# Kernel optimization log

Hardware: AMD Instinct MI355X
Metric: run time of the kernel (lower is better)

## Reference

```python
import jax, jax.numpy as jnp
import numpy as np

EPS = 1e-5


def _bn_relu(y, g, beta, relu=True):
    # BatchNorm1d in training mode: biased batch stats over (B, V) per channel
    mean = jnp.mean(y, axis=(0, 2), keepdims=True)
    var = jnp.mean((y - mean) ** 2, axis=(0, 2), keepdims=True)
    out = (y - mean) * jax.lax.rsqrt(var + EPS) * g[None, :, None] + beta[None, :, None]
    return jnp.maximum(out, 0.0) if relu else out


def _spiral_conv(x, idx, w, b, g, beta):
    # x: (B,C,V), idx: (V,L) -> gather (B,C,V,L), row-major reshape to (B,C*L,V)
    B, C, V = x.shape
    L = idx.shape[1]
    neigh = x[:, :, idx].reshape(B, C * L, V)
    y = jnp.einsum('om,bmv->bov', w, neigh) + b[None, :, None]
    return _bn_relu(y, g, beta)


def _se(x, w1, w2):
    s = jnp.mean(x, axis=2)                              # (B,C)
    h = jnp.maximum(jnp.einsum('bc,rc->br', s, w1), 0.0)  # (B,r)
    s = jax.nn.sigmoid(jnp.einsum('br,cr->bc', h, w2))   # (B,C)
    return x * s[:, :, None]


def setup_inputs() -> dict:
    key = jax.random.key(0)
    ks = jax.random.split(key, 24)
    B, V, L, H = 2, 16384, 12, 256
    sc = 0.05
    inp = {
        'verts': jax.random.normal(ks[0], (B, V, 3), jnp.float32),
        'spirals': jax.random.randint(ks[1], (4, V, L), 0, V, jnp.int32),
        'enc0_w': jax.random.normal(ks[2], (H, 3 * L), jnp.float32) * sc,
        'enc0_b': jax.random.normal(ks[3], (H,), jnp.float32) * sc,
        'enc0_g': jnp.ones((H,), jnp.float32),
        'enc0_beta': jnp.zeros((H,), jnp.float32),
        'enc_w': jax.random.normal(ks[4], (3, H, H * L), jnp.float32) * sc,
        'enc_b': jax.random.normal(ks[5], (3, H), jnp.float32) * sc,
        'enc_g': jnp.ones((3, H), jnp.float32),
        'enc_beta': jnp.zeros((3, H), jnp.float32),
        'se_w1': jax.random.normal(ks[6], (4, H // 8, H), jnp.float32) * sc,
        'se_w2': jax.random.normal(ks[7], (4, H, H // 8), jnp.float32) * sc,
        'skip_w': jax.random.normal(ks[8], (3, H, 2 * H), jnp.float32) * sc,
        'skip_b': jax.random.normal(ks[9], (3, H), jnp.float32) * sc,
        'dec_w': jax.random.normal(ks[10], (3, H, H * L), jnp.float32) * sc,
        'dec_b': jax.random.normal(ks[11], (3, H), jnp.float32) * sc,
        'dec_g': jnp.ones((3, H), jnp.float32),
        'dec_beta': jnp.zeros((3, H), jnp.float32),
        'cls1_w': jax.random.normal(ks[12], (H // 2, H), jnp.float32) * sc,
        'cls1_b': jax.random.normal(ks[13], (H // 2,), jnp.float32) * sc,
        'cls1_g': jnp.ones((H // 2,), jnp.float32),
        'cls1_beta': jnp.zeros((H // 2,), jnp.float32),
        'cls2_w': jax.random.normal(ks[14], (H // 4, H // 2), jnp.float32) * sc,
        'cls2_b': jax.random.normal(ks[15], (H // 4,), jnp.float32) * sc,
        'cls2_g': jnp.ones((H // 4,), jnp.float32),
        'cls2_beta': jnp.zeros((H // 4,), jnp.float32),
        'cls3_w': jax.random.normal(ks[16], (1, H // 4), jnp.float32) * sc,
        'cls3_b': jax.random.normal(ks[17], (1,), jnp.float32) * sc,
    }
    return inp


def reference(verts, spirals, enc0_w, enc0_b, enc0_g, enc0_beta,
              enc_w, enc_b, enc_g, enc_beta, se_w1, se_w2,
              skip_w, skip_b, dec_w, dec_b, dec_g, dec_beta,
              cls1_w, cls1_b, cls1_g, cls1_beta,
              cls2_w, cls2_b, cls2_g, cls2_beta, cls3_w, cls3_b):
    x = jnp.transpose(verts, (0, 2, 1))  # (B,3,V)
    feats = []
    # encoder: 4 blocks, block0 has no residual (3 != 256)
    for i in range(4):
        if i == 0:
            out = _spiral_conv(x, spirals[0], enc0_w, enc0_b, enc0_g, enc0_beta)
        else:
            out = _spiral_conv(x, spirals[i], enc_w[i - 1], enc_b[i - 1], enc_g[i - 1], enc_beta[i - 1]) + x
        x = _se(out, se_w1[i], se_w2[i])
        feats.append(x)
    # decoder with skip-concat fusion, spirals[2],[1],[0] and feats[2],[1],[0]
    for i in range(3):
        feat = feats[2 - i]
        idx = spirals[2 - i]
        xc = jnp.concatenate([x, feat], axis=1)  # (B,512,V)
        x = jnp.einsum('oc,bcv->bov', skip_w[i], xc) + skip_b[i][None, :, None]
        x = _spiral_conv(x, idx, dec_w[i], dec_b[i], dec_g[i], dec_beta[i]) + x
    # classifier: 1x1 conv stack
    h = _bn_relu(jnp.einsum('oc,bcv->bov', cls1_w, x) + cls1_b[None, :, None], cls1_g, cls1_beta)
    h = _bn_relu(jnp.einsum('oc,bcv->bov', cls2_w, h) + cls2_b[None, :, None], cls2_g, cls2_beta)
    out = jnp.einsum('oc,bcv->bov', cls3_w, h) + cls3_b[None, :, None]  # (B,1,V)
    return out[:, 0, :]  # (B,V)
```

## Files before the change

kernel.cpp:

```cpp
#include <hip/hip_runtime.h>

typedef unsigned short u16;
using f16x8 = __attribute__((ext_vector_type(8))) _Float16;
using f32x4 = __attribute__((ext_vector_type(4))) float;

#define V_N 16384
#define M_N 32768

__device__ __forceinline__ float h2f(u16 u) {
  _Float16 h; __builtin_memcpy(&h, &u, 2); return (float)h;
}
__device__ __forceinline__ u16 f2h(float f) {
  _Float16 h = (_Float16)f; u16 u; __builtin_memcpy(&u, &h, 2); return u;
}

__device__ __forceinline__ void dma16(const u16* g, u16* l) {
  __builtin_amdgcn_global_load_lds(
      (const __attribute__((address_space(1))) void*)(const void*)g,
      (__attribute__((address_space(3))) void*)(void*)l, 16, 0, 0);
}

__global__ __launch_bounds__(256) void perm2_k(const float* __restrict__ w, u16* __restrict__ wp) {
  int o = blockIdx.x & 255, layer = blockIdx.x >> 8;
  int t = threadIdx.x;
  const float* src = w + ((size_t)layer * 256 + o) * 3072;
  u16* dst = wp + (size_t)layer * 786432;
  float2 v[6];
  #pragma unroll
  for (int q = 0; q < 6; ++q) v[q] = *(const float2*)(src + t * 12 + q * 2);
  const float* vf = (const float*)v;
  int lo = t & 31;
  #pragma unroll
  for (int m = 0; m < 12; ++m) {
    int kc = m * 8 + (t >> 5);
    dst[(size_t)kc * 8192 + o * 32 + lo] = f2h(vf[m]);
  }
}

__global__ __launch_bounds__(256) void permfr_k(const float* __restrict__ src, u16* __restrict__ dst,
                                                int O, int K) {
  int i = blockIdx.x * 256 + threadIdx.x;
  if (i >= (K << 8)) return;
  int j = i & 7, lq = (i >> 3) & 3, col = (i >> 5) & 255, kc = i >> 13;
  int k = kc * 32 + lq * 8 + j;
  float v = (col < O) ? src[(size_t)col * K + k] : 0.f;
  dst[i] = f2h(v);
}

__global__ __launch_bounds__(256) void wscale_k(const u16* __restrict__ w, const float* __restrict__ sig,
                                                const float* __restrict__ sigx,
                                                u16* __restrict__ o, int n, int sel) {
  int i = blockIdx.x * 256 + threadIdx.x;
  if (i >= n) return;
  float wv = h2f(w[i]);
  int k = (i >> 13) * 32 + ((i >> 3) & 3) * 8 + (i & 7);
  int c = k & 255;
  #pragma unroll
  for (int b = 0; b < 2; ++b) {
    float s;
    if (sel == 511 && k < 256) s = sigx ? sigx[b * 256 + c] : 1.f;
    else                       s = sig[b * 256 + c];
    o[(long)b * n + i] = f2h(wv * s);
  }
}

__global__ __launch_bounds__(256) void enc0_k(const float* __restrict__ verts, const int* __restrict__ sp,
                                              const float* __restrict__ w0, u16* __restrict__ y) {
  __shared__ float xs[32][36];
  int t = threadIdx.x;
  int r0 = blockIdx.x * 32;
  for (int s = t; s < 32 * 12; s += 256) {
    int row = s / 12, tt = s - row * 12;
    int gr = r0 + row;
    int b = gr >> 14, v = gr & (V_N - 1);
    int j = sp[tt * V_N + v];
    const float* p = verts + ((long)b * V_N + j) * 3;
    xs[row][tt]      = p[0];
    xs[row][12 + tt] = p[1];
    xs[row][24 + tt] = p[2];
  }
  __syncthreads();
  float w[36];
  #pragma unroll
  for (int k = 0; k < 36; ++k) w[k] = w0[t * 36 + k];
  for (int row = 0; row < 32; ++row) {
    float a = 0.f;
    #pragma unroll
    for (int k = 0; k < 36; ++k) a += w[k] * xs[row][k];
    y[(long)(r0 + row) * 256 + t] = f2h(a);
  }
}

template<int CT>
__global__ __launch_bounds__(512, 4) void gemm3_k(
    const u16* __restrict__ P0, const u16* __restrict__ P1, int lda,
    const int* __restrict__ sp, int L,
    const u16* __restrict__ Wt, long wstride,
    u16* __restrict__ Yb, const float* __restrict__ bias, int Ostore,
    float* __restrict__ stats)
{
  constexpr int KC   = CT >> 5;
  constexpr int PH   = (CT == 256) ? 4 : 2;
  constexpr int KCP  = KC / PH;
  constexpr int PROW = 64;
  constexpr int BUFE = 64 * PROW;
  __shared__ __align__(16) u16 lA[3 * BUFE];
  const int tid  = threadIdx.x;
  const int wave = tid >> 6, lane = tid & 63;
  const int wn = wave * 32;
  const int lr = lane & 15, lq = lane >> 4;
  const int nwg = gridDim.x;
  const int wg = (blockIdx.x & 7) * (nwg >> 3) + (blockIdx.x >> 3);
  const int bm = wg * 64;
  const int batch = bm >> 14;
  const int vbase = bm & (V_N - 1);
  const int qrow = lane >> 3;
  const int qchunk = lane & 7;
  const bool gat = (sp != nullptr);
  const long rowb = (long)batch * V_N;
  const u16* Pd1 = P1 ? P1 : P0;
  const u16* Wb = Wt + (long)batch * wstride;
  const int NS = PH * L;

  const u16* bp[2];
  #pragma unroll
  for (int nt = 0; nt < 2; ++nt)
    bp[nt] = Wb + ((long)(wn + nt * 16 + lr) * 4 + lq) * 8;

  auto load_idx = [&](int tap) -> int {
    int v = 0;
    if (gat && lane < 8) v = sp[(long)tap * V_N + vbase + wave * 8 + lane];
    return v;
  };

  auto dma_st = [&](u16* buf, const u16* src, int idxreg, int ph) {
    u16* wb = buf + wave * (8 * PROW);
    int rloc = wave * 8 + qrow;
    long grow;
    if (gat) grow = rowb + (long)__shfl(idxreg, qrow, 64);
    else     grow = bm + rloc;
    const u16* gp = src + grow * lda + ph * PROW + ((qchunk ^ (rloc & 7)) << 3);
    dma16(gp, wb);
  };

  auto loadB = [&](int cb, f16x8 (&tB)[KCP * 2]) {
    #pragma unroll
    for (int kp = 0; kp < KCP; ++kp)
      #pragma unroll
      for (int nt = 0; nt < 2; ++nt)
        tB[kp * 2 + nt] = *(const f16x8*)(bp[nt] + (long)(cb + kp) * 8192);
  };

  f32x4 acc[4][2];
  #pragma unroll
  for (int i = 0; i < 4; ++i)
    #pragma unroll
    for (int j = 0; j < 2; ++j) acc[i][j] = (f32x4){0.f, 0.f, 0.f, 0.f};

  auto compute_st = [&](const u16* buf, const f16x8 (&tB)[KCP * 2]) {
    #pragma unroll
    for (int kp = 0; kp < KCP; ++kp) {
      f16x8 a[4];
      #pragma unroll
      for (int mt = 0; mt < 4; ++mt) {
        int row = mt * 16 + lr;
        a[mt] = *(const f16x8*)(&buf[row * PROW + (((kp * 4 + lq) ^ (row & 7)) << 3)]);
      }
      #pragma unroll
      for (int mt = 0; mt < 4; ++mt)
        #pragma unroll
        for (int nt = 0; nt < 2; ++nt)
          acc[mt][nt] = __builtin_amdgcn_mfma_f32_16x16x32_f16(a[mt], tB[kp * 2 + nt], acc[mt][nt], 0, 0, 0);
    }
  };

  f16x8 tA[KCP * 2], tB2[KCP * 2];

  auto adv = [&](int& l, int& ph) { if (++l == L) { l = 0; ++ph; } };
  int lB = 0, phB = 0; adv(lB, phB);
  int lD = lB, phD = phB; adv(lD, phD);
  int lI = lD; { int pT = phD; int lT = lI; adv(lT, pT); lI = lT; }
  int idxN;

  {
    int i0 = load_idx(0);
    int i1 = load_idx(lB);
    idxN = load_idx(lD);
    dma_st(lA, P0, i0, 0);
    if (NS > 1) {
      const u16* s1 = (!gat && lB > 0) ? Pd1 : P0;
      dma_st(lA + BUFE, s1, i1, phB);
    }
    __builtin_amdgcn_sched_barrier(0);
    loadB(0, tA);
    __builtin_amdgcn_sched_barrier(0);
  }

  auto stage = [&](int s, f16x8 (&tCur)[KCP * 2], f16x8 (&tNxt)[KCP * 2]) {
    if (s + 1 < NS) asm volatile("s_waitcnt vmcnt(5)" ::: "memory");
    else            asm volatile("s_waitcnt vmcnt(0)" ::: "memory");
    asm volatile("s_waitcnt lgkmcnt(0)" ::: "memory");
    __builtin_amdgcn_s_barrier();
    __builtin_amdgcn_sched_barrier(0);
    if (s + 1 < NS) loadB(lB * KC + phB * KCP, tNxt);
    __builtin_amdgcn_sched_barrier(0);
    int idxT = 0;
    if (gat && s + 3 < NS) idxT = load_idx(lI);
    if (s + 2 < NS) {
      const u16* srcD = (!gat && lD > 0) ? Pd1 : P0;
      dma_st(lA + ((s + 2) % 3) * BUFE, srcD, idxN, phD);
    }
    __builtin_amdgcn_sched_barrier(0);
    compute_st(lA + (s % 3) * BUFE, tCur);
    adv(lB, phB); adv(lD, phD); if (++lI == L) lI = 0;
    idxN = idxT;
  };

  for (int s = 0; s < NS; s += 2) {
    stage(s, tA, tB2);
    stage(s + 1, tB2, tA);
  }

  #pragma unroll
  for (int nt = 0; nt < 2; ++nt) {
    int col = wn + nt * 16 + lr;
    if (col < Ostore) {
      float bv = bias ? bias[col] : 0.f;
      float s1 = 0.f, s2 = 0.f;
      #pragma unroll
      for (int mt = 0; mt < 4; ++mt) {
        #pragma unroll
        for (int rg = 0; rg < 4; ++rg) {
          int row = bm + mt * 16 + lq * 4 + rg;
          float v = acc[mt][nt][rg] + bv;
          Yb[(long)row * Ostore + col] = f2h(v);
          s1 += v; s2 += v * v;
        }
      }
      if (stats) {
        s1 += __shfl_xor(s1, 16); s1 += __shfl_xor(s1, 32);
        s2 += __shfl_xor(s2, 16); s2 += __shfl_xor(s2, 32);
        if (lq == 0) {
          atomicAdd(&stats[col], s1);
          atomicAdd(&stats[Ostore + col], s2);
        }
      }
    }
  }
}

__global__ __launch_bounds__(256) void stats2_k(const u16* __restrict__ y, float* __restrict__ st) {
  __shared__ float s1L[256], s2L[256];
  int tid = threadIdx.x;
  int ci = (tid & 63) * 4;
  int r0 = blockIdx.x * 64 + (tid >> 6);
  float a1[4] = {0,0,0,0}, a2[4] = {0,0,0,0};
  for (int it = 0; it < 16; ++it) {
    long i = ((long)r0 + it * 4) * 256 + ci;
    uint2 pv = *(const uint2*)(y + i);
    float v0 = h2f((u16)(pv.x & 0xffff)), v1 = h2f((u16)(pv.x >> 16));
    float v2 = h2f((u16)(pv.y & 0xffff)), v3 = h2f((u16)(pv.y >> 16));
    a1[0] += v0; a1[1] += v1; a1[2] += v2; a1[3] += v3;
    a2[0] += v0*v0; a2[1] += v1*v1; a2[2] += v2*v2; a2[3] += v3*v3;
  }
  s1L[tid] = 0.f; s2L[tid] = 0.f;
  __syncthreads();
  #pragma unroll
  for (int j = 0; j < 4; ++j) { atomicAdd(&s1L[ci + j], a1[j]); atomicAdd(&s2L[ci + j], a2[j]); }
  __syncthreads();
  atomicAdd(&st[tid], s1L[tid]);
  atomicAdd(&st[256 + tid], s2L[tid]);
}

__global__ __launch_bounds__(256) void bnrelu2_k(
    const u16* __restrict__ y, const float* __restrict__ st,
    const float* __restrict__ g, const float* __restrict__ be,
    const u16* __restrict__ resid, const float* __restrict__ rscale,
    u16* __restrict__ ob, float* __restrict__ ses, int O)
{
  __shared__ float sL[256];
  int tid = threadIdx.x;
  int tpr = O >> 2;
  int rpi = 256 / tpr;
  int ci = (tid & (tpr - 1)) * 4;
  int row0 = blockIdx.x * (rpi * 16);
  int r0 = row0 + (tid / tpr);
  int b = row0 >> 14;
  float mean[4], sc[4], sh[4], rs[4];
  #pragma unroll
  for (int j = 0; j < 4; ++j) {
    int c = ci + j;
    float m = st[c] * (1.f / 32768.f);
    float var = st[O + c] * (1.f / 32768.f) - m * m;
    mean[j] = m;
    sc[j] = rsqrtf(fmaxf(var, 0.f) + 1e-5f) * g[c];
    sh[j] = be[c];
    rs[j] = rscale ? rscale[b * 256 + c] : 1.f;
  }
  float ss[4] = {0,0,0,0};
  for (int it = 0; it < 16; ++it) {
    long i = ((long)r0 + (long)it * rpi) * O + ci;
    uint2 pv = *(const uint2*)(y + i);
    float v[4];
    v[0] = fmaxf((h2f((u16)(pv.x & 0xffff)) - mean[0]) * sc[0] + sh[0], 0.f);
    v[1] = fmaxf((h2f((u16)(pv.x >> 16))    - mean[1]) * sc[1] + sh[1], 0.f);
    v[2] = fmaxf((h2f((u16)(pv.y & 0xffff)) - mean[2]) * sc[2] + sh[2], 0.f);
    v[3] = fmaxf((h2f((u16)(pv.y >> 16))    - mean[3]) * sc[3] + sh[3], 0.f);
    if (resid) {
      uint2 rv = *(const uint2*)(resid + i);
      v[0] += h2f((u16)(rv.x & 0xffff)) * rs[0]; v[1] += h2f((u16)(rv.x >> 16)) * rs[1];
      v[2] += h2f((u16)(rv.y & 0xffff)) * rs[2]; v[3] += h2f((u16)(rv.y >> 16)) * rs[3];
    }
    uint2 pk;
    pk.x = (unsigned)f2h(v[0]) | ((unsigned)f2h(v[1]) << 16);
    pk.y = (unsigned)f2h(v[2]) | ((unsigned)f2h(v[3]) << 16);
    *(uint2*)(ob + i) = pk;
    #pragma unroll
    for (int j = 0; j < 4; ++j) ss[j] += v[j];
  }
  if (ses) {
    sL[tid] = 0.f;
    __syncthreads();
    #pragma unroll
    for (int j = 0; j < 4; ++j) atomicAdd(&sL[ci + j], ss[j]);
    __syncthreads();
    atomicAdd(&ses[b * O + tid], sL[tid]);
  }
}

__global__ void se_k(const float* __restrict__ ses, const float* __restrict__ w1,
                     const float* __restrict__ w2, float* __restrict__ sig)
{
  __shared__ float s[256];
  __shared__ float h[32];
  int b = blockIdx.x, t = threadIdx.x;
  s[t] = ses[b * 256 + t] * (1.f / 16384.f);
  __syncthreads();
  if (t < 32) {
    float a = 0.f;
    for (int c = 0; c < 256; ++c) a += w1[t * 256 + c] * s[c];
    h[t] = fmaxf(a, 0.f);
  }
  __syncthreads();
  float a = 0.f;
  #pragma unroll
  for (int r = 0; r < 32; ++r) a += w2[t * 32 + r] * h[r];
  sig[b * 256 + t] = 1.f / (1.f + expf(-a));
}

__global__ __launch_bounds__(256) void cls3_k(const u16* __restrict__ h2, const float* __restrict__ w,
                                              const float* __restrict__ b, float* __restrict__ out)
{
  __shared__ float ws[64];
  int t = threadIdx.x;
  if (t < 64) ws[t] = w[t];
  __syncthreads();
  int r = blockIdx.x * 256 + t;
  const u16* p = h2 + (long)r * 64;
  float a = b[0];
  #pragma unroll
  for (int c = 0; c < 64; ++c) a += ws[c] * h2f(p[c]);
  out[r] = a;
}

extern "C" void kernel_launch(void* const* d_in, const int* in_sizes, int n_in,
                              void* d_out, int out_size, void* d_ws, size_t ws_size,
                              hipStream_t stream)
{
  (void)in_sizes; (void)n_in; (void)out_size; (void)ws_size;
  const float* verts   = (const float*)d_in[0];
  const int*   spirals = (const int*)d_in[1];
  const float* enc0_w  = (const float*)d_in[2];
  const float* enc0_g  = (const float*)d_in[4];
  const float* enc0_be = (const float*)d_in[5];
  const float* enc_w   = (const float*)d_in[6];
  const float* enc_g   = (const float*)d_in[8];
  const float* enc_be  = (const float*)d_in[9];
  const float* se_w1   = (const float*)d_in[10];
  const float* se_w2   = (const float*)d_in[11];
  const float* skip_w  = (const float*)d_in[12];
  const float* skip_b  = (const float*)d_in[13];
  const float* dec_w   = (const float*)d_in[14];
  const float* dec_g   = (const float*)d_in[16];
  const float* dec_be  = (const float*)d_in[17];
  const float* cls1_w  = (const float*)d_in[18];
  const float* cls1_g  = (const float*)d_in[20];
  const float* cls1_be = (const float*)d_in[21];
  const float* cls2_w  = (const float*)d_in[22];
  const float* cls2_g  = (const float*)d_in[24];
  const float* cls2_be = (const float*)d_in[25];
  const float* cls3_w  = (const float*)d_in[26];
  const float* cls3_b  = (const float*)d_in[27];

  char* p = (char*)d_ws;
  auto alloc = [&](size_t n) { char* q = p; p += (n + 255) & ~(size_t)255; return q; };
  u16* wpe     = (u16*)alloc((size_t)6 * 256 * 3072 * 2);
  u16* wpe_s   = (u16*)alloc((size_t)3 * 2 * 256 * 3072 * 2);
  u16* skip_wb = (u16*)alloc((size_t)3 * 256 * 512 * 2);
  u16* skip_s  = (u16*)alloc((size_t)3 * 2 * 256 * 512 * 2);
  u16* cls1_wb = (u16*)alloc((size_t)256 * 256 * 2);
  u16* wp6     = (u16*)alloc((size_t)256 * 128 * 2);
  float* stats = (float*)alloc(2048);
  float* sesum = (float*)alloc(2048);
  float* sig   = (float*)alloc(4 * 2048);
  u16* out0 = (u16*)alloc((size_t)M_N * 256 * 2);
  u16* out1 = (u16*)alloc((size_t)M_N * 256 * 2);
  u16* out2 = (u16*)alloc((size_t)M_N * 256 * 2);
  u16* ct   = (u16*)alloc((size_t)M_N * 256 * 2);
  u16* tb   = (u16*)alloc((size_t)M_N * 256 * 2);
  u16* xd   = (u16*)alloc((size_t)M_N * 256 * 2);
  u16* outs[4] = {out0, out1, out2, ct};
  const size_t WENC = (size_t)256 * 3072;
  const size_t WSKP = (size_t)256 * 512;

  perm2_k<<<768, 256, 0, stream>>>(enc_w, wpe);
  perm2_k<<<768, 256, 0, stream>>>(dec_w, wpe + (size_t)3 * WENC);
  for (int s = 0; s < 3; ++s)
    permfr_k<<<512, 256, 0, stream>>>(skip_w + (size_t)s * 256 * 512,
                                      skip_wb + (size_t)s * WSKP, 256, 512);
  permfr_k<<<256, 256, 0, stream>>>(cls1_w, cls1_wb, 128, 256);
  permfr_k<<<128, 256, 0, stream>>>(cls2_w, wp6, 64, 128);

  hipMemsetAsync(stats, 0, 4096, stream);
  enc0_k<<<1024, 256, 0, stream>>>(verts, spirals, enc0_w, ct);
  stats2_k<<<512, 256, 0, stream>>>(ct, stats);
  bnrelu2_k<<<512, 256, 0, stream>>>(ct, stats, enc0_g, enc0_be, nullptr, nullptr, out0, sesum, 256);
  se_k<<<2, 256, 0, stream>>>(sesum, se_w1, se_w2, sig);

  for (int i = 1; i < 4; ++i) {
    wscale_k<<<3072, 256, 0, stream>>>(wpe + (size_t)(i - 1) * WENC, sig + (i - 1) * 512, nullptr,
                                       wpe_s + (size_t)(i - 1) * 2 * WENC, (int)WENC, 255);
    hipMemsetAsync(stats, 0, 4096, stream);
    gemm3_k<256><<<512, 512, 0, stream>>>(outs[i - 1], nullptr, 256,
                                          spirals + (size_t)i * V_N * 12, 12,
                                          wpe_s + (size_t)(i - 1) * 2 * WENC, (long)WENC,
                                          ct, nullptr, 256, stats);
    bnrelu2_k<<<512, 256, 0, stream>>>(ct, stats, enc_g + (i - 1) * 256, enc_be + (i - 1) * 256,
                                       outs[i - 1], sig + (i - 1) * 512, outs[i], sesum, 256);
    se_k<<<2, 256, 0, stream>>>(sesum, se_w1 + (size_t)i * 32 * 256,
                                se_w2 + (size_t)i * 256 * 32, sig + i * 512);
  }

  for (int i = 0; i < 3; ++i) {
    wscale_k<<<512, 256, 0, stream>>>(skip_wb + (size_t)i * WSKP, sig + (2 - i) * 512,
                                      (i == 0) ? (sig + 3 * 512) : nullptr,
                                      skip_s + (size_t)i * 2 * WSKP, (int)WSKP, 511);
    gemm3_k<256><<<512, 512, 0, stream>>>((i == 0) ? ct : xd, outs[2 - i], 256, nullptr, 2,
                                          skip_s + (size_t)i * 2 * WSKP, (long)WSKP,
                                          tb, skip_b + i * 256, 256, nullptr);
    hipMemsetAsync(stats, 0, 4096, stream);
    gemm3_k<256><<<512, 512, 0, stream>>>(tb, nullptr, 256,
                                          spirals + (size_t)(2 - i) * V_N * 12, 12,
                                          wpe + (size_t)(3 + i) * WENC, 0,
                                          outs[2 - i], nullptr, 256, stats);
    bnrelu2_k<<<512, 256, 0, stream>>>(outs[2 - i], stats, dec_g + i * 256, dec_be + i * 256,
                                       tb, nullptr, xd, nullptr, 256);
  }

  hipMemsetAsync(stats, 0, 4096, stream);
  gemm3_k<256><<<512, 512, 0, stream>>>(xd, nullptr, 256, nullptr, 1,
                                        cls1_wb, 0, ct, nullptr, 128, stats);
  bnrelu2_k<<<256, 256, 0, stream>>>(ct, stats, cls1_g, cls1_be, nullptr, nullptr, ct, nullptr, 128);
  hipMemsetAsync(stats, 0, 4096, stream);
  gemm3_k<128><<<512, 512, 0, stream>>>(ct, nullptr, 128, nullptr, 1,
                                        wp6, 0, tb, nullptr, 64, stats);
  bnrelu2_k<<<128, 256, 0, stream>>>(tb, stats, cls2_g, cls2_be, nullptr, nullptr, tb, nullptr, 64);
  cls3_k<<<128, 256, 0, stream>>>(tb, cls3_w, cls3_b, (float*)d_out);
}
```

Baseline: 884.5 us.

## Pair taps per GEMM stage, fuse SE and BN stats, drop memsets

The GEMM now processes two spiral taps per pipeline stage, giving each barrier twice the work and fewer stages. It loads the B fragments inline per stage, precomputes the LDS offsets and raises wave priority around the MFMA bursts. BN statistics for enc0 move into enc0_k, and the SE MLP is folded into bnrelu2_k through a last-block counter. Per-layer stats buffers replace the repeated memsets, cutting launches and serialisation. In exchange the larger LDS buffers may lower occupancy, and the inline B loads are no longer prefetched a stage ahead, which can expose global latency.

```diff
diff --git a/kernel.cpp b/kernel.cpp
--- a/kernel.cpp
+++ b/kernel.cpp
@@ -65,7 +65,8 @@
 }
 
 __global__ __launch_bounds__(256) void enc0_k(const float* __restrict__ verts, const int* __restrict__ sp,
-                                              const float* __restrict__ w0, u16* __restrict__ y) {
+                                              const float* __restrict__ w0, u16* __restrict__ y,
+                                              float* __restrict__ st) {
   __shared__ float xs[32][36];
   int t = threadIdx.x;
   int r0 = blockIdx.x * 32;
@@ -83,15 +84,21 @@
   float w[36];
   #pragma unroll
   for (int k = 0; k < 36; ++k) w[k] = w0[t * 36 + k];
+  float s1 = 0.f, s2 = 0.f;
   for (int row = 0; row < 32; ++row) {
     float a = 0.f;
     #pragma unroll
     for (int k = 0; k < 36; ++k) a += w[k] * xs[row][k];
-    y[(long)(r0 + row) * 256 + t] = f2h(a);
-  }
-}
-
-template<int CT>
+    u16 h = f2h(a);
+    y[(long)(r0 + row) * 256 + t] = h;
+    float av = h2f(h);
+    s1 += av; s2 += av * av;
+  }
+  atomicAdd(&st[t], s1);
+  atomicAdd(&st[256 + t], s2);
+}
+
+template<int CT, int TPS>
 __global__ __launch_bounds__(512, 4) void gemm3_k(
     const u16* __restrict__ P0, const u16* __restrict__ P1, int lda,
     const int* __restrict__ sp, int L,
@@ -104,7 +111,9 @@
   constexpr int KCP  = KC / PH;
   constexpr int PROW = 64;
   constexpr int BUFE = 64 * PROW;
-  __shared__ __align__(16) u16 lA[3 * BUFE];
+  constexpr int SBUF = TPS * BUFE;
+  constexpr int NB   = TPS * KCP * 2;
+  __shared__ __align__(16) u16 lA[3 * SBUF];
   const int tid  = threadIdx.x;
   const int wave = tid >> 6, lane = tid & 63;
   const int wn = wave * 32;
@@ -120,105 +129,114 @@
   const long rowb = (long)batch * V_N;
   const u16* Pd1 = P1 ? P1 : P0;
   const u16* Wb = Wt + (long)batch * wstride;
-  const int NS = PH * L;
+  const int NP = L / TPS;
+  const int NS = PH * NP;
 
   const u16* bp[2];
   #pragma unroll
   for (int nt = 0; nt < 2; ++nt)
     bp[nt] = Wb + ((long)(wn + nt * 16 + lr) * 4 + lq) * 8;
 
-  auto load_idx = [&](int tap) -> int {
+  int aOff[4][2];
+  #pragma unroll
+  for (int mt = 0; mt < 4; ++mt)
+    #pragma unroll
+    for (int kp = 0; kp < 2; ++kp) {
+      int row = mt * 16 + lr;
+      aOff[mt][kp] = row * PROW + (((kp * 4 + lq) ^ (row & 7)) << 3);
+    }
+
+  auto load_idxp = [&](int p) -> int {
     int v = 0;
-    if (gat && lane < 8) v = sp[(long)tap * V_N + vbase + wave * 8 + lane];
+    if (gat && lane < 8 * TPS) {
+      int t = p * TPS + (lane >> 3);
+      v = sp[(long)t * V_N + vbase + wave * 8 + (lane & 7)];
+    }
     return v;
   };
 
-  auto dma_st = [&](u16* buf, const u16* src, int idxreg, int ph) {
-    u16* wb = buf + wave * (8 * PROW);
-    int rloc = wave * 8 + qrow;
-    long grow;
-    if (gat) grow = rowb + (long)__shfl(idxreg, qrow, 64);
-    else     grow = bm + rloc;
-    const u16* gp = src + grow * lda + ph * PROW + ((qchunk ^ (rloc & 7)) << 3);
-    dma16(gp, wb);
+  auto dma_pair = [&](u16* buf, int p, int ph, int idxreg) {
+    #pragma unroll
+    for (int i = 0; i < TPS; ++i) {
+      const u16* src = gat ? P0 : ((p * TPS + i) > 0 ? Pd1 : P0);
+      u16* wb = buf + i * BUFE + wave * (8 * PROW);
+      int rloc = wave * 8 + qrow;
+      long grow;
+      if (gat) grow = rowb + (long)__shfl(idxreg, i * 8 + qrow, 64);
+      else     grow = bm + rloc;
+      const u16* gp = src + grow * lda + ph * PROW + ((qchunk ^ (rloc & 7)) << 3);
+      dma16(gp, wb);
+    }
   };
 
-  auto loadB = [&](int cb, f16x8 (&tB)[KCP * 2]) {
-    #pragma unroll
-    for (int kp = 0; kp < KCP; ++kp)
-      #pragma unroll
-      for (int nt = 0; nt < 2; ++nt)
-        tB[kp * 2 + nt] = *(const f16x8*)(bp[nt] + (long)(cb + kp) * 8192);
-  };
-
   f32x4 acc[4][2];
   #pragma unroll
   for (int i = 0; i < 4; ++i)
     #pragma unroll
     for (int j = 0; j < 2; ++j) acc[i][j] = (f32x4){0.f, 0.f, 0.f, 0.f};
 
-  auto compute_st = [&](const u16* buf, const f16x8 (&tB)[KCP * 2]) {
-    #pragma unroll
-    for (int kp = 0; kp < KCP; ++kp) {
-      f16x8 a[4];
-      #pragma unroll
-      for (int mt = 0; mt < 4; ++mt) {
-        int row = mt * 16 + lr;
-        a[mt] = *(const f16x8*)(&buf[row * PROW + (((kp * 4 + lq) ^ (row & 7)) << 3)]);
-      }
-      #pragma unroll
-      for (int mt = 0; mt < 4; ++mt)
-        #pragma unroll
-        for (int nt = 0; nt < 2; ++nt)
-          acc[mt][nt] = __builtin_amdgcn_mfma_f32_16x16x32_f16(a[mt], tB[kp * 2 + nt], acc[mt][nt], 0, 0, 0);
-    }
-  };
-
-  f16x8 tA[KCP * 2], tB2[KCP * 2];
-
-  auto adv = [&](int& l, int& ph) { if (++l == L) { l = 0; ++ph; } };
-  int lB = 0, phB = 0; adv(lB, phB);
-  int lD = lB, phD = phB; adv(lD, phD);
-  int lI = lD; { int pT = phD; int lT = lI; adv(lT, pT); lI = lT; }
   int idxN;
-
   {
-    int i0 = load_idx(0);
-    int i1 = load_idx(lB);
-    idxN = load_idx(lD);
-    dma_st(lA, P0, i0, 0);
-    if (NS > 1) {
-      const u16* s1 = (!gat && lB > 0) ? Pd1 : P0;
-      dma_st(lA + BUFE, s1, i1, phB);
-    }
+    int i0 = load_idxp(0);
+    int i1 = load_idxp(1 % NP);
+    idxN   = load_idxp(2 % NP);
     __builtin_amdgcn_sched_barrier(0);
-    loadB(0, tA);
+    dma_pair(lA, 0, 0, i0);
+    if (NS > 1) dma_pair(lA + SBUF, 1 % NP, 1 / NP, i1);
     __builtin_amdgcn_sched_barrier(0);
   }
 
-  auto stage = [&](int s, f16x8 (&tCur)[KCP * 2], f16x8 (&tNxt)[KCP * 2]) {
-    if (s + 1 < NS) asm volatile("s_waitcnt vmcnt(5)" ::: "memory");
+  int pC = 0, phC = 0;
+  int pD = 2 % NP, phD = 2 / NP;
+  int pI = 3 % NP;
+  int bC = 0, bD = 2;
+
+  for (int s = 0; s < NS; ++s) {
+    if (s + 1 < NS) asm volatile("s_waitcnt vmcnt(2)" ::: "memory");
     else            asm volatile("s_waitcnt vmcnt(0)" ::: "memory");
     asm volatile("s_waitcnt lgkmcnt(0)" ::: "memory");
     __builtin_amdgcn_s_barrier();
     __builtin_amdgcn_sched_barrier(0);
-    if (s + 1 < NS) loadB(lB * KC + phB * KCP, tNxt);
+    f16x8 tB[NB];
+    #pragma unroll
+    for (int i = 0; i < TPS; ++i)
+      #pragma unroll
+      for (int kp = 0; kp < KCP; ++kp)
+        #pragma unroll
+        for (int nt = 0; nt < 2; ++nt)
+          tB[(i * KCP + kp) * 2 + nt] =
+            *(const f16x8*)(bp[nt] + (long)((pC * TPS + i) * KC + phC * KCP + kp) * 8192);
     __builtin_amdgcn_sched_barrier(0);
     int idxT = 0;
-    if (gat && s + 3 < NS) idxT = load_idx(lI);
-    if (s + 2 < NS) {
-      const u16* srcD = (!gat && lD > 0) ? Pd1 : P0;
-      dma_st(lA + ((s + 2) % 3) * BUFE, srcD, idxN, phD);
-    }
+    if (gat && s + 3 < NS) idxT = load_idxp(pI);
+    if (s + 2 < NS) dma_pair(lA + bD * SBUF, pD, phD, idxN);
     __builtin_amdgcn_sched_barrier(0);
-    compute_st(lA + (s % 3) * BUFE, tCur);
-    adv(lB, phB); adv(lD, phD); if (++lI == L) lI = 0;
+    #pragma unroll
+    for (int i = 0; i < TPS; ++i) {
+      const int toff = bC * SBUF + i * BUFE;
+      #pragma unroll
+      for (int kp = 0; kp < KCP; ++kp) {
+        f16x8 a[4];
+        #pragma unroll
+        for (int mt = 0; mt < 4; ++mt)
+          a[mt] = *(const f16x8*)(lA + toff + aOff[mt][kp]);
+        __builtin_amdgcn_sched_barrier(0);
+        __builtin_amdgcn_s_setprio(1);
+        #pragma unroll
+        for (int mt = 0; mt < 4; ++mt) {
+          acc[mt][0] = __builtin_amdgcn_mfma_f32_16x16x32_f16(a[mt], tB[(i * KCP + kp) * 2 + 0], acc[mt][0], 0, 0, 0);
+          acc[mt][1] = __builtin_amdgcn_mfma_f32_16x16x32_f16(a[mt], tB[(i * KCP + kp) * 2 + 1], acc[mt][1], 0, 0, 0);
+        }
+        __builtin_amdgcn_s_setprio(0);
+        __builtin_amdgcn_sched_barrier(0);
+      }
+    }
+    if (++pC == NP) { pC = 0; ++phC; }
+    if (++pD == NP) { pD = 0; ++phD; }
+    if (++pI == NP) { pI = 0; }
+    bC = (bC == 2) ? 0 : bC + 1;
+    bD = (bD == 2) ? 0 : bD + 1;
     idxN = idxT;
-  };
-
-  for (int s = 0; s < NS; s += 2) {
-    stage(s, tA, tB2);
-    stage(s + 1, tB2, tA);
   }
 
   #pragma unroll
@@ -249,36 +267,17 @@
   }
 }
 
-__global__ __launch_bounds__(256) void stats2_k(const u16* __restrict__ y, float* __restrict__ st) {
-  __shared__ float s1L[256], s2L[256];
-  int tid = threadIdx.x;
-  int ci = (tid & 63) * 4;
-  int r0 = blockIdx.x * 64 + (tid >> 6);
-  float a1[4] = {0,0,0,0}, a2[4] = {0,0,0,0};
-  for (int it = 0; it < 16; ++it) {
-    long i = ((long)r0 + it * 4) * 256 + ci;
-    uint2 pv = *(const uint2*)(y + i);
-    float v0 = h2f((u16)(pv.x & 0xffff)), v1 = h2f((u16)(pv.x >> 16));
-    float v2 = h2f((u16)(pv.y & 0xffff)), v3 = h2f((u16)(pv.y >> 16));
-    a1[0] += v0; a1[1] += v1; a1[2] += v2; a1[3] += v3;
-    a2[0] += v0*v0; a2[1] += v1*v1; a2[2] += v2*v2; a2[3] += v3*v3;
-  }
-  s1L[tid] = 0.f; s2L[tid] = 0.f;
-  __syncthreads();
-  #pragma unroll
-  for (int j = 0; j < 4; ++j) { atomicAdd(&s1L[ci + j], a1[j]); atomicAdd(&s2L[ci + j], a2[j]); }
-  __syncthreads();
-  atomicAdd(&st[tid], s1L[tid]);
-  atomicAdd(&st[256 + tid], s2L[tid]);
-}
-
 __global__ __launch_bounds__(256) void bnrelu2_k(
     const u16* __restrict__ y, const float* __restrict__ st,
     const float* __restrict__ g, const float* __restrict__ be,
     const u16* __restrict__ resid, const float* __restrict__ rscale,
-    u16* __restrict__ ob, float* __restrict__ ses, int O)
+    u16* __restrict__ ob, float* __restrict__ ses, int O,
+    const float* __restrict__ sw1, const float* __restrict__ sw2,
+    float* __restrict__ sig, int* __restrict__ cnt)
 {
   __shared__ float sL[256];
+  __shared__ float hh[32];
+  __shared__ int lastFlag;
   int tid = threadIdx.x;
   int tpr = O >> 2;
   int rpi = 256 / tpr;
@@ -325,27 +324,31 @@
     for (int j = 0; j < 4; ++j) atomicAdd(&sL[ci + j], ss[j]);
     __syncthreads();
     atomicAdd(&ses[b * O + tid], sL[tid]);
-  }
-}
-
-__global__ void se_k(const float* __restrict__ ses, const float* __restrict__ w1,
-                     const float* __restrict__ w2, float* __restrict__ sig)
-{
-  __shared__ float s[256];
-  __shared__ float h[32];
-  int b = blockIdx.x, t = threadIdx.x;
-  s[t] = ses[b * 256 + t] * (1.f / 16384.f);
-  __syncthreads();
-  if (t < 32) {
-    float a = 0.f;
-    for (int c = 0; c < 256; ++c) a += w1[t * 256 + c] * s[c];
-    h[t] = fmaxf(a, 0.f);
-  }
-  __syncthreads();
-  float a = 0.f;
-  #pragma unroll
-  for (int r = 0; r < 32; ++r) a += w2[t * 32 + r] * h[r];
-  sig[b * 256 + t] = 1.f / (1.f + expf(-a));
+    if (sw1) {
+      __threadfence();
+      __syncthreads();
+      if (tid == 0) {
+        int r = atomicAdd(&cnt[b], 1);
+        lastFlag = (r == 255);
+      }
+      __syncthreads();
+      if (lastFlag) {
+        __threadfence();
+        sL[tid] = ses[b * 256 + tid] * (1.f / 16384.f);
+        __syncthreads();
+        if (tid < 32) {
+          float a = 0.f;
+          for (int c = 0; c < 256; ++c) a += sw1[tid * 256 + c] * sL[c];
+          hh[tid] = fmaxf(a, 0.f);
+        }
+        __syncthreads();
+        float a = 0.f;
+        #pragma unroll
+        for (int r = 0; r < 32; ++r) a += sw2[tid * 32 + r] * hh[r];
+        sig[b * 256 + tid] = 1.f / (1.f + expf(-a));
+      }
+    }
+  }
 }
 
 __global__ __launch_bounds__(256) void cls3_k(const u16* __restrict__ h2, const float* __restrict__ w,
@@ -400,8 +403,9 @@
   u16* skip_s  = (u16*)alloc((size_t)3 * 2 * 256 * 512 * 2);
   u16* cls1_wb = (u16*)alloc((size_t)256 * 256 * 2);
   u16* wp6     = (u16*)alloc((size_t)256 * 128 * 2);
-  float* stats = (float*)alloc(2048);
-  float* sesum = (float*)alloc(2048);
+  float* stats = (float*)alloc(10 * 2048);
+  float* sesum = (float*)alloc(4 * 2048);
+  int*   cnt   = (int*)alloc(256);
   float* sig   = (float*)alloc(4 * 2048);
   u16* out0 = (u16*)alloc((size_t)M_N * 256 * 2);
   u16* out1 = (u16*)alloc((size_t)M_N * 256 * 2);
@@ -413,6 +417,8 @@
   const size_t WENC = (size_t)256 * 3072;
   const size_t WSKP = (size_t)256 * 512;
 
+  hipMemsetAsync(stats, 0, 10 * 2048 + 4 * 2048 + 256, stream);
+
   perm2_k<<<768, 256, 0, stream>>>(enc_w, wpe);
   perm2_k<<<768, 256, 0, stream>>>(dec_w, wpe + (size_t)3 * WENC);
   for (int s = 0; s < 3; ++s)
@@ -421,49 +427,46 @@
   permfr_k<<<256, 256, 0, stream>>>(cls1_w, cls1_wb, 128, 256);
   permfr_k<<<128, 256, 0, stream>>>(cls2_w, wp6, 64, 128);
 
-  hipMemsetAsync(stats, 0, 4096, stream);
-  enc0_k<<<1024, 256, 0, stream>>>(verts, spirals, enc0_w, ct);
-  stats2_k<<<512, 256, 0, stream>>>(ct, stats);
-  bnrelu2_k<<<512, 256, 0, stream>>>(ct, stats, enc0_g, enc0_be, nullptr, nullptr, out0, sesum, 256);
-  se_k<<<2, 256, 0, stream>>>(sesum, se_w1, se_w2, sig);
+  enc0_k<<<1024, 256, 0, stream>>>(verts, spirals, enc0_w, ct, stats);
+  bnrelu2_k<<<512, 256, 0, stream>>>(ct, stats, enc0_g, enc0_be, nullptr, nullptr,
+                                     out0, sesum, 256, se_w1, se_w2, sig, cnt);
 
   for (int i = 1; i < 4; ++i) {
     wscale_k<<<3072, 256, 0, stream>>>(wpe + (size_t)(i - 1) * WENC, sig + (i - 1) * 512, nullptr,
                                        wpe_s + (size_t)(i - 1) * 2 * WENC, (int)WENC, 255);
-    hipMemsetAsync(stats, 0, 4096, stream);
-    gemm3_k<256><<<512, 512, 0, stream>>>(outs[i - 1], nullptr, 256,
-                                          spirals + (size_t)i * V_N * 12, 12,
-                                          wpe_s + (size_t)(i - 1) * 2 * WENC, (long)WENC,
-                                          ct, nullptr, 256, stats);
-    bnrelu2_k<<<512, 256, 0, stream>>>(ct, stats, enc_g + (i - 1) * 256, enc_be + (i - 1) * 256,
-                                       outs[i - 1], sig + (i - 1) * 512, outs[i], sesum, 256);
-    se_k<<<2, 256, 0, stream>>>(sesum, se_w1 + (size_t)i * 32 * 256,
-                                se_w2 + (size_t)i * 256 * 32, sig + i * 512);
+    gemm3_k<256, 2><<<512, 512, 0, stream>>>(outs[i - 1], nullptr, 256,
+                                             spirals + (size_t)i * V_N * 12, 12,
+                                             wpe_s + (size_t)(i - 1) * 2 * WENC, (long)WENC,
+                                             ct, nullptr, 256, stats + i * 512);
+    bnrelu2_k<<<512, 256, 0, stream>>>(ct, stats + i * 512, enc_g + (i - 1) * 256, enc_be + (i - 1) * 256,
+                                       outs[i - 1], sig + (i - 1) * 512, outs[i], sesum + i * 512, 256,
+                                       se_w1 + (size_t)i * 32 * 256, se_w2 + (size_t)i * 256 * 32,
+                                       sig + i * 512, cnt + i * 2);
   }
 
   for (int i = 0; i < 3; ++i) {
     wscale_k<<<512, 256, 0, stream>>>(skip_wb + (size_t)i * WSKP, sig + (2 - i) * 512,
                                       (i == 0) ? (sig + 3 * 512) : nullptr,
                                       skip_s + (size_t)i * 2 * WSKP, (int)WSKP, 511);
-    gemm3_k<256><<<512, 512, 0, stream>>>((i == 0) ? ct : xd, outs[2 - i], 256, nullptr, 2,
-                                          skip_s + (size_t)i * 2 * WSKP, (long)WSKP,
-                                          tb, skip_b + i * 256, 256, nullptr);
-    hipMemsetAsync(stats, 0, 4096, stream);
-    gemm3_k<256><<<512, 512, 0, stream>>>(tb, nullptr, 256,
-                                          spirals + (size_t)(2 - i) * V_N * 12, 12,
-                                          wpe + (size_t)(3 + i) * WENC, 0,
-                                          outs[2 - i], nullptr, 256, stats);
-    bnrelu2_k<<<512, 256, 0, stream>>>(outs[2 - i], stats, dec_g + i * 256, dec_be + i * 256,
-                                       tb, nullptr, xd, nullptr, 256);
-  }
-
-  hipMemsetAsync(stats, 0, 4096, stream);
-  gemm3_k<256><<<512, 512, 0, stream>>>(xd, nullptr, 256, nullptr, 1,
-                                        cls1_wb, 0, ct, nullptr, 128, stats);
-  bnrelu2_k<<<256, 256, 0, stream>>>(ct, stats, cls1_g, cls1_be, nullptr, nullptr, ct, nullptr, 128);
-  hipMemsetAsync(stats, 0, 4096, stream);
-  gemm3_k<128><<<512, 512, 0, stream>>>(ct, nullptr, 128, nullptr, 1,
-                                        wp6, 0, tb, nullptr, 64, stats);
-  bnrelu2_k<<<128, 256, 0, stream>>>(tb, stats, cls2_g, cls2_be, nullptr, nullptr, tb, nullptr, 64);
+    gemm3_k<256, 2><<<512, 512, 0, stream>>>((i == 0) ? ct : xd, outs[2 - i], 256, nullptr, 2,
+                                             skip_s + (size_t)i * 2 * WSKP, (long)WSKP,
+                                             tb, skip_b + i * 256, 256, nullptr);
+    gemm3_k<256, 2><<<512, 512, 0, stream>>>(tb, nullptr, 256,
+                                             spirals + (size_t)(2 - i) * V_N * 12, 12,
+                                             wpe + (size_t)(3 + i) * WENC, 0,
+                                             outs[2 - i], nullptr, 256, stats + (4 + i) * 512);
+    bnrelu2_k<<<512, 256, 0, stream>>>(outs[2 - i], stats + (4 + i) * 512, dec_g + i * 256, dec_be + i * 256,
+                                       tb, nullptr, xd, nullptr, 256,
+                                       nullptr, nullptr, nullptr, nullptr);
+  }
+
+  gemm3_k<256, 1><<<512, 512, 0, stream>>>(xd, nullptr, 256, nullptr, 1,
+                                           cls1_wb, 0, ct, nullptr, 128, stats + 7 * 512);
+  bnrelu2_k<<<256, 256, 0, stream>>>(ct, stats + 7 * 512, cls1_g, cls1_be, nullptr, nullptr,
+                                     ct, nullptr, 128, nullptr, nullptr, nullptr, nullptr);
+  gemm3_k<128, 1><<<512, 512, 0, stream>>>(ct, nullptr, 128, nullptr, 1,
+                                           wp6, 0, tb, nullptr, 64, stats + 8 * 512);
+  bnrelu2_k<<<128, 256, 0, stream>>>(tb, stats + 8 * 512, cls2_g, cls2_be, nullptr, nullptr,
+                                     tb, nullptr, 64, nullptr, nullptr, nullptr, nullptr);
   cls3_k<<<128, 256, 0, stream>>>(tb, cls3_w, cls3_b, (float*)d_out);
 }
```

New measurement: 1.392 ms. +57.4%, slower.
